# Kernel tuning notes

Hardware: AMD Instinct MI355X
Metric: run time of the kernel (lower is better)

## Reference

```python
import jax, jax.numpy as jnp
import numpy as np

B, C, L = 32, 128, 256  # batch, channels (graph nodes), temporal features (= feas)
K = 2  # Chebyshev order (hardcoded in the module)


def setup_inputs() -> dict:
    key = jax.random.key(0)
    k1, k2, k3 = jax.random.split(key, 3)
    x = jax.random.normal(k1, (B, C, L), dtype=jnp.float32)
    a = jax.random.uniform(k2, (C, C), dtype=jnp.float32)  # nn.Parameter(torch.rand)
    Theta = jax.random.normal(k3, (K, L, L), dtype=jnp.float32)  # (k, feas, num_of_filters)
    return {"x": x, "a": a, "Theta": Theta}


def reference(x, a, Theta):
    b, c, l = x.shape
    # pairwise L1 distance over the feature axis: diff[b,i,j] = sum_l |x[b,i,l] - x[b,j,l]|
    diff = jnp.abs(x[:, :, None, :] - x[:, None, :, :]).sum(-1)  # [b,c,c]
    # F.normalize(diff, dim=0): L2-normalize across the batch dimension
    norm = jnp.sqrt((diff * diff).sum(axis=0, keepdims=True))
    diff = diff / jnp.maximum(norm, 1e-12)
    # learned adjacency
    tmpS = jnp.exp(jax.nn.relu((1.0 - diff) * a))        # [b,c,c]
    adj = tmpS / tmpS.sum(axis=1, keepdims=True)
    deg = adj.sum(axis=1)                                 # [b,c]
    I = jnp.eye(c, dtype=x.dtype)
    D = deg[:, :, None] * I                               # diag_embed(deg)
    Lap = D - adj
    lambda_max = 2.0
    L_t = 2.0 * Lap / lambda_max - I                      # scaled Laplacian, [b,c,c]
    cheb = [jnp.broadcast_to(I, (b, c, c)), L_t]
    for i in range(2, K):
        cheb.append(2.0 * L_t * cheb[i - 1] - cheb[i - 2])
    out = jnp.zeros((b, c, Theta.shape[2]), dtype=x.dtype)
    for kk in range(K):
        # rhs = bmm(T_k^T, x): rhs[b,j,l] = sum_i T_k[b,i,j] * x[b,i,l]
        rhs = jnp.einsum('bij,bil->bjl', cheb[kk], x)
        out = out + rhs @ Theta[kk]
    return jax.nn.relu(out)
```

## Files before the change

### kernel.cpp

```cpp
#include <hip/hip_runtime.h>
#include <hip/hip_bf16.h>


#define NB 32
#define NC 128
#define NL 256

typedef short bf16x8 __attribute__((ext_vector_type(8)));
typedef float f32x4 __attribute__((ext_vector_type(4)));

static __device__ __forceinline__ unsigned short f2bf(float f) {
    unsigned u = __builtin_bit_cast(unsigned, f);
    u += 0x7fff + ((u >> 16) & 1);
    return (unsigned short)(u >> 16);
}

__device__ const unsigned char TI36[36] = {0,0,0,0,0,0,0,0, 1,1,1,1,1,1,1, 2,2,2,2,2,2,
                                           3,3,3,3,3, 4,4,4,4, 5,5,5, 6,6, 7};
__device__ const unsigned char TJ36[36] = {0,1,2,3,4,5,6,7, 1,2,3,4,5,6,7, 2,3,4,5,6,7,
                                           3,4,5,6,7, 4,5,6,7, 5,6,7, 6,7, 7};

__global__ __launch_bounds__(256) void k_pre(const float* __restrict__ x,
                                             const float* __restrict__ Theta,
                                             const float* __restrict__ a,
                                             float* __restrict__ diff,
                                             unsigned short* __restrict__ xb,
                                             unsigned short* __restrict__ thT,
                                             float* __restrict__ aT) {
    __shared__ float smem[8592];
    int bid = blockIdx.x;
    int tid = threadIdx.x;

    if (bid < 1152) {
        int b = bid / 36, p = bid - b * 36;
        int i0 = TI36[p] * 16, j0 = TJ36[p] * 16;
        float* xi = smem;
        float* xj = smem + 4160;
        float* sT = smem + 8320;
        const float4* x4 = (const float4*)(x + (size_t)b * NC * NL);
        for (int idx = tid; idx < 16 * 64; idx += 256) {
            int r = idx >> 6, c = idx & 63;
            *(float4*)&xi[r * 260 + c * 4] = x4[(i0 + r) * 64 + c];
            *(float4*)&xj[r * 260 + c * 4] = x4[(j0 + r) * 64 + c];
        }
        __syncthreads();
        int il = tid >> 4, jl = tid & 15;
        float acc = 0.f;
        #pragma unroll 8
        for (int l4 = 0; l4 < 64; ++l4) {
            float4 u = *(const float4*)&xi[il * 260 + l4 * 4];
            float4 v = *(const float4*)&xj[jl * 260 + l4 * 4];
            acc += fabsf(u.x - v.x) + fabsf(u.y - v.y) +
                   fabsf(u.z - v.z) + fabsf(u.w - v.w);
        }
        float* D = diff + (size_t)b * NC * NC;
        D[(i0 + il) * NC + j0 + jl] = acc;
        sT[jl * 17 + il] = acc;
        __syncthreads();
        D[(j0 + il) * NC + i0 + jl] = sT[il * 17 + jl];
    } else if (bid < 2176) {
        int idx = (bid - 1152) * 256 + tid;
        float4 v = ((const float4*)x)[idx];
        ushort4 o;
        o.x = f2bf(v.x); o.y = f2bf(v.y); o.z = f2bf(v.z); o.w = f2bf(v.w);
        ((ushort4*)xb)[idx] = o;
    } else if (bid < 2208) {
        int tt = bid - 2176;
        int t = tt >> 4, rem = tt & 15;
        int l0 = (rem >> 2) * 64, n0 = (rem & 3) * 64;
        const float* Tp = Theta + (size_t)t * 65536;
        for (int it = tid; it < 4096; it += 256) {
            int r = it >> 6, c = it & 63;
            smem[r * 65 + c] = Tp[(l0 + r) * 256 + n0 + c];
        }
        __syncthreads();
        for (int it = tid; it < 4096; it += 256) {
            int r = it >> 6, c = it & 63;
            thT[(size_t)(t * 256 + n0 + r) * 256 + l0 + c] = f2bf(smem[c * 65 + r]);
        }
    } else {
        int tt = bid - 2208;
        int i0 = (tt >> 1) * 64, j0 = (tt & 1) * 64;
        for (int it = tid; it < 4096; it += 256) {
            int r = it >> 6, c = it & 63;
            smem[r * 65 + c] = a[(i0 + r) * NC + j0 + c];
        }
        __syncthreads();
        for (int it = tid; it < 4096; it += 256) {
            int r = it >> 6, c = it & 63;
            aT[(j0 + r) * NC + i0 + c] = smem[c * 65 + r];
        }
    }
}

__global__ __launch_bounds__(128) void k_adj(const float* __restrict__ diff,
                                             const float* __restrict__ aT,
                                             unsigned short* __restrict__ adjTb) {
    int bid = blockIdx.x;
    int b = bid >> 7, j = bid & 127;
    int i = threadIdx.x;
    const float* Dj = diff + j * NC + i;
    float ss = 0.f;
    #pragma unroll
    for (int bb = 0; bb < NB; ++bb) {
        float v = Dj[(size_t)bb * NC * NC];
        ss = fmaf(v, v, ss);
    }
    float rn = 1.0f / fmaxf(sqrtf(ss), 1e-12f);
    float d  = Dj[(size_t)b * NC * NC];
    float av = aT[j * NC + i];
    float s = __expf(fmaxf((1.0f - d * rn) * av, 0.0f));
    float t = s;
    #pragma unroll
    for (int off = 32; off; off >>= 1) t += __shfl_xor(t, off);
    __shared__ float partial[2];
    if ((i & 63) == 0) partial[i >> 6] = t;
    __syncthreads();
    float total = partial[0] + partial[1];
    adjTb[(size_t)b * NC * NC + j * NC + i] = f2bf(s / total);
}

__global__ __launch_bounds__(256) void k_xth(const unsigned short* __restrict__ xb,
                                             const unsigned short* __restrict__ thT,
                                             float* __restrict__ xTh0,
                                             unsigned short* __restrict__ xTh1T) {
    __shared__ unsigned short Bs[8192];
    int bid = blockIdx.x;
    int mt = bid >> 4, nt = bid & 15;
    int m0 = mt * 128, n0 = nt * 32;
    int tid = threadIdx.x, w = tid >> 6, lane = tid & 63;
    int lr = lane & 15, lg = lane >> 4;

    #pragma unroll
    for (int it = 0; it < 4; ++it) {
        int c = tid + it * 256;
        int n = c >> 5, kc = c & 31;
        bf16x8 v = *(const bf16x8*)(thT + (size_t)(n0 + n) * 256 + kc * 8);
        int dst = n * 512 + ((kc * 16) ^ ((n & 7) << 4));
        *(bf16x8*)((char*)Bs + dst) = v;
    }
    __syncthreads();

    const unsigned short* Ap0 = xb + (size_t)(m0 + w * 32 + lr) * 256 + lg * 8;
    const unsigned short* Ap1 = Ap0 + 16 * 256;
    f32x4 acc00 = {0.f,0.f,0.f,0.f}, acc01 = {0.f,0.f,0.f,0.f};
    f32x4 acc10 = {0.f,0.f,0.f,0.f}, acc11 = {0.f,0.f,0.f,0.f};
    int swz = (lr & 7) << 4;
    #pragma unroll
    for (int ks = 0; ks < 8; ++ks) {
        bf16x8 a0 = *(const bf16x8*)(Ap0 + ks * 32);
        bf16x8 a1 = *(const bf16x8*)(Ap1 + ks * 32);
        int kb = (ks * 64 + lg * 16) ^ swz;
        bf16x8 b0 = *(const bf16x8*)((char*)Bs + lr * 512 + kb);
        bf16x8 b1 = *(const bf16x8*)((char*)Bs + (16 + lr) * 512 + kb);
        acc00 = __builtin_amdgcn_mfma_f32_16x16x32_bf16(a0, b0, acc00, 0, 0, 0);
        acc01 = __builtin_amdgcn_mfma_f32_16x16x32_bf16(a0, b1, acc01, 0, 0, 0);
        acc10 = __builtin_amdgcn_mfma_f32_16x16x32_bf16(a1, b0, acc10, 0, 0, 0);
        acc11 = __builtin_amdgcn_mfma_f32_16x16x32_bf16(a1, b1, acc11, 0, 0, 0);
    }

    int ir0 = w * 32 + lg * 4;
    if (n0 < 256) {
        float* O = xTh0 + (size_t)mt * 32768 + (size_t)ir0 * 256 + n0 + lr;
        #pragma unroll
        for (int r = 0; r < 4; ++r) {
            O[r * 256]              = acc00[r];
            O[r * 256 + 16]         = acc01[r];
            O[(16 + r) * 256]       = acc10[r];
            O[(16 + r) * 256 + 16]  = acc11[r];
        }
    } else {
        int n1 = n0 - 256;
        unsigned short* O = xTh1T + (size_t)mt * 32768;
        ushort4 p;
        p.x = f2bf(acc00[0]); p.y = f2bf(acc00[1]); p.z = f2bf(acc00[2]); p.w = f2bf(acc00[3]);
        *(ushort4*)(O + (size_t)(n1 + lr) * 128 + ir0) = p;
        p.x = f2bf(acc01[0]); p.y = f2bf(acc01[1]); p.z = f2bf(acc01[2]); p.w = f2bf(acc01[3]);
        *(ushort4*)(O + (size_t)(n1 + 16 + lr) * 128 + ir0) = p;
        p.x = f2bf(acc10[0]); p.y = f2bf(acc10[1]); p.z = f2bf(acc10[2]); p.w = f2bf(acc10[3]);
        *(ushort4*)(O + (size_t)(n1 + lr) * 128 + ir0 + 16) = p;
        p.x = f2bf(acc11[0]); p.y = f2bf(acc11[1]); p.z = f2bf(acc11[2]); p.w = f2bf(acc11[3]);
        *(ushort4*)(O + (size_t)(n1 + 16 + lr) * 128 + ir0 + 16) = p;
    }
}

__global__ __launch_bounds__(256) void k_out(const unsigned short* __restrict__ adjTb,
                                             const unsigned short* __restrict__ xTh1T,
                                             const float* __restrict__ xTh0,
                                             float* __restrict__ out) {
    int bid = blockIdx.x;
    int b = bid >> 4, t16 = bid & 15;
    int j0 = (t16 >> 3) * 64, n0 = (t16 & 7) * 32;
    int tid = threadIdx.x, w = tid >> 6, lane = tid & 63;
    int lr = lane & 15, lg = lane >> 4;
    const unsigned short* Ap  = adjTb + (size_t)b * 16384 + (size_t)(j0 + w * 16 + lr) * 128 + lg * 8;
    const unsigned short* Bp0 = xTh1T + (size_t)b * 32768 + (size_t)(n0 + lr) * 128 + lg * 8;
    const unsigned short* Bp1 = Bp0 + 16 * 128;
    f32x4 acc0 = {0.f,0.f,0.f,0.f}, acc1 = {0.f,0.f,0.f,0.f};
    #pragma unroll
    for (int ks = 0; ks < 4; ++ks) {
        bf16x8 av = *(const bf16x8*)(Ap + ks * 32);
        bf16x8 b0 = *(const bf16x8*)(Bp0 + ks * 32);
        bf16x8 b1 = *(const bf16x8*)(Bp1 + ks * 32);
        acc0 = __builtin_amdgcn_mfma_f32_16x16x32_bf16(av, b0, acc0, 0, 0, 0);
        acc1 = __builtin_amdgcn_mfma_f32_16x16x32_bf16(av, b1, acc1, 0, 0, 0);
    }
    int j = j0 + w * 16 + lg * 4;
    const float* X0 = xTh0 + (size_t)b * 32768 + (size_t)j * 256 + n0 + lr;
    float* O = out + (size_t)b * 32768 + (size_t)j * 256 + n0 + lr;
    #pragma unroll
    for (int r = 0; r < 4; ++r) {
        O[r * 256]      = fmaxf(X0[r * 256]      - acc0[r], 0.f);
        O[r * 256 + 16] = fmaxf(X0[r * 256 + 16] - acc1[r], 0.f);
    }
}

extern "C" void kernel_launch(void* const* d_in, const int* in_sizes, int n_in,
                              void* d_out, int out_size, void* d_ws, size_t ws_size,
                              hipStream_t stream) {
    const float* x     = (const float*)d_in[0];
    const float* a     = (const float*)d_in[1];
    const float* Theta = (const float*)d_in[2];
    float* out = (float*)d_out;
    float* f0  = (float*)d_ws;

    float*          diff  = f0;
    unsigned short* xTh1T = (unsigned short*)f0;
    float*          aT    = f0 + 524288;
    float*          xTh0  = f0 + 540672;
    unsigned short* xb    = (unsigned short*)(f0 + 1589248);
    unsigned short* thT   = (unsigned short*)(f0 + 2113536);
    unsigned short* adjTb = (unsigned short*)(f0 + 2179072);

    k_pre<<<dim3(2212), dim3(256), 0, stream>>>(x, Theta, a, diff, xb, thT, aT);
    k_adj<<<dim3(NB * NC), dim3(128), 0, stream>>>(diff, aT, adjTb);
    k_xth<<<dim3(512), dim3(256), 0, stream>>>(xb, thT, xTh0, xTh1T);
    k_out<<<dim3(512), dim3(256), 0, stream>>>(adjTb, xTh1T, xTh0, out);
}
```

Baseline: 92.30 us.

## Fuse all stages into one cooperative persistent kernel with grid syncs

Replaces the four kernel launches with a single cooperative kernel of 512 blocks. It loops over the preprocessing jobs, then separates the adjacency, x·Theta GEMM and output GEMM stages with grid.sync. The per-column batch norm is now computed once into a new rnorm buffer, where each adjacency block used to recompute it by reading all 32 batches of diff. The diff tile load is split into two halves so shared memory fits two blocks per CU. The cost is grid-wide barrier overhead and a fixed grid size, which serialises the preprocessing jobs across blocks.

Result: slower. 335.1 us (+263.0%).

```diff
diff --git a/kernel.cpp b/kernel.cpp
--- a/kernel.cpp
+++ b/kernel.cpp
@@ -1,10 +1,14 @@
 #include <hip/hip_runtime.h>
 #include <hip/hip_bf16.h>
+#include <hip/hip_cooperative_groups.h>
+
+namespace cg = cooperative_groups;
 
 
 #define NB 32
 #define NC 128
 #define NL 256
+#define GRID 512
 
 typedef short bf16x8 __attribute__((ext_vector_type(8)));
 typedef float f32x4 __attribute__((ext_vector_type(4)));
@@ -20,198 +24,209 @@
 __device__ const unsigned char TJ36[36] = {0,1,2,3,4,5,6,7, 1,2,3,4,5,6,7, 2,3,4,5,6,7,
                                            3,4,5,6,7, 4,5,6,7, 5,6,7, 6,7, 7};
 
-__global__ __launch_bounds__(256) void k_pre(const float* __restrict__ x,
-                                             const float* __restrict__ Theta,
-                                             const float* __restrict__ a,
-                                             float* __restrict__ diff,
-                                             unsigned short* __restrict__ xb,
-                                             unsigned short* __restrict__ thT,
-                                             float* __restrict__ aT) {
-    __shared__ float smem[8592];
-    int bid = blockIdx.x;
-    int tid = threadIdx.x;
-
-    if (bid < 1152) {
-        int b = bid / 36, p = bid - b * 36;
-        int i0 = TI36[p] * 16, j0 = TJ36[p] * 16;
-        float* xi = smem;
-        float* xj = smem + 4160;
-        float* sT = smem + 8320;
-        const float4* x4 = (const float4*)(x + (size_t)b * NC * NL);
-        for (int idx = tid; idx < 16 * 64; idx += 256) {
-            int r = idx >> 6, c = idx & 63;
-            *(float4*)&xi[r * 260 + c * 4] = x4[(i0 + r) * 64 + c];
-            *(float4*)&xj[r * 260 + c * 4] = x4[(j0 + r) * 64 + c];
+__global__ __launch_bounds__(256, 2) void k_fused(
+    const float* __restrict__ x, const float* __restrict__ Theta, const float* __restrict__ a,
+    float* __restrict__ diff, unsigned short* __restrict__ xb, unsigned short* __restrict__ thT,
+    float* __restrict__ aT, float* __restrict__ rnorm, unsigned short* __restrict__ adjTb,
+    float* __restrict__ xTh0, unsigned short* __restrict__ xTh1T, float* __restrict__ out)
+{
+    cg::grid_group grid = cg::this_grid();
+    __shared__ __align__(16) float smem[4496];
+    __shared__ float partial[4];
+    int bid = blockIdx.x, tid = threadIdx.x;
+
+    for (int job = bid; job < 2212; job += GRID) {
+        if (job < 1152) {
+            int b = job / 36, p = job - b * 36;
+            int i0 = TI36[p] * 16, j0 = TJ36[p] * 16;
+            float* xi = smem;
+            float* xj = smem + 2112;
+            float* sT = smem + 4224;
+            const float4* x4 = (const float4*)(x + (size_t)b * NC * NL);
+            int il = tid >> 4, jl = tid & 15;
+            float acc = 0.f;
+            #pragma unroll
+            for (int h = 0; h < 2; ++h) {
+                __syncthreads();
+                for (int idx = tid; idx < 512; idx += 256) {
+                    int r = idx >> 5, c = idx & 31;
+                    *(float4*)&xi[r * 132 + c * 4] = x4[(i0 + r) * 64 + h * 32 + c];
+                    *(float4*)&xj[r * 132 + c * 4] = x4[(j0 + r) * 64 + h * 32 + c];
+                }
+                __syncthreads();
+                #pragma unroll 8
+                for (int l4 = 0; l4 < 32; ++l4) {
+                    float4 u = *(const float4*)&xi[il * 132 + l4 * 4];
+                    float4 v = *(const float4*)&xj[jl * 132 + l4 * 4];
+                    acc += fabsf(u.x - v.x) + fabsf(u.y - v.y) +
+                           fabsf(u.z - v.z) + fabsf(u.w - v.w);
+                }
+            }
+            float* D = diff + (size_t)b * NC * NC;
+            D[(i0 + il) * NC + j0 + jl] = acc;
+            __syncthreads();
+            sT[jl * 17 + il] = acc;
+            __syncthreads();
+            D[(j0 + il) * NC + i0 + jl] = sT[il * 17 + jl];
+        } else if (job < 2176) {
+            int idx = (job - 1152) * 256 + tid;
+            float4 v = ((const float4*)x)[idx];
+            ushort4 o;
+            o.x = f2bf(v.x); o.y = f2bf(v.y); o.z = f2bf(v.z); o.w = f2bf(v.w);
+            ((ushort4*)xb)[idx] = o;
+        } else if (job < 2208) {
+            int tt = job - 2176;
+            int t = tt >> 4, rem = tt & 15;
+            int l0 = (rem >> 2) * 64, n0 = (rem & 3) * 64;
+            const float* Tp = Theta + (size_t)t * 65536;
+            __syncthreads();
+            for (int it = tid; it < 4096; it += 256) {
+                int r = it >> 6, c = it & 63;
+                smem[r * 65 + c] = Tp[(l0 + r) * 256 + n0 + c];
+            }
+            __syncthreads();
+            for (int it = tid; it < 4096; it += 256) {
+                int r = it >> 6, c = it & 63;
+                thT[(size_t)(t * 256 + n0 + r) * 256 + l0 + c] = f2bf(smem[c * 65 + r]);
+            }
+        } else {
+            int tt = job - 2208;
+            int i0 = (tt >> 1) * 64, j0 = (tt & 1) * 64;
+            __syncthreads();
+            for (int it = tid; it < 4096; it += 256) {
+                int r = it >> 6, c = it & 63;
+                smem[r * 65 + c] = a[(i0 + r) * NC + j0 + c];
+            }
+            __syncthreads();
+            for (int it = tid; it < 4096; it += 256) {
+                int r = it >> 6, c = it & 63;
+                aT[(j0 + r) * NC + i0 + c] = smem[c * 65 + r];
+            }
+        }
+    }
+    grid.sync();
+
+    if (bid < 64) {
+        int idx = bid * 256 + tid;
+        float ss = 0.f;
+        #pragma unroll
+        for (int bb = 0; bb < NB; ++bb) {
+            float v = diff[(size_t)bb * NC * NC + idx];
+            ss = fmaf(v, v, ss);
+        }
+        rnorm[idx] = 1.0f / fmaxf(sqrtf(ss), 1e-12f);
+    }
+    grid.sync();
+
+    {
+        int g = tid >> 7;
+        int i = tid & 127;
+        #pragma unroll
+        for (int it = 0; it < 4; ++it) {
+            __syncthreads();
+            int P = it * 1024 + bid * 2 + g;
+            int b = P >> 7, j = P & 127;
+            float d  = diff[(size_t)b * NC * NC + j * NC + i];
+            float rn = rnorm[j * NC + i];
+            float av = aT[j * NC + i];
+            float s = __expf(fmaxf((1.0f - d * rn) * av, 0.0f));
+            float t = s;
+            #pragma unroll
+            for (int off = 32; off; off >>= 1) t += __shfl_xor(t, off);
+            if ((tid & 63) == 0) partial[tid >> 6] = t;
+            __syncthreads();
+            float total = partial[g << 1] + partial[(g << 1) | 1];
+            adjTb[(size_t)b * NC * NC + j * NC + i] = f2bf(s / total);
+        }
+    }
+    grid.sync();
+
+    {
+        unsigned short* Bs = (unsigned short*)smem;
+        int mt = bid >> 4, nt = bid & 15;
+        int m0 = mt * 128, n0 = nt * 32;
+        int w = tid >> 6, lane = tid & 63;
+        int lr = lane & 15, lg = lane >> 4;
+
+        #pragma unroll
+        for (int it = 0; it < 4; ++it) {
+            int c = tid + it * 256;
+            int n = c >> 5, kc = c & 31;
+            bf16x8 v = *(const bf16x8*)(thT + (size_t)(n0 + n) * 256 + kc * 8);
+            int dst = n * 512 + ((kc * 16) ^ ((n & 7) << 4));
+            *(bf16x8*)((char*)Bs + dst) = v;
         }
         __syncthreads();
-        int il = tid >> 4, jl = tid & 15;
-        float acc = 0.f;
-        #pragma unroll 8
-        for (int l4 = 0; l4 < 64; ++l4) {
-            float4 u = *(const float4*)&xi[il * 260 + l4 * 4];
-            float4 v = *(const float4*)&xj[jl * 260 + l4 * 4];
-            acc += fabsf(u.x - v.x) + fabsf(u.y - v.y) +
-                   fabsf(u.z - v.z) + fabsf(u.w - v.w);
-        }
-        float* D = diff + (size_t)b * NC * NC;
-        D[(i0 + il) * NC + j0 + jl] = acc;
-        sT[jl * 17 + il] = acc;
-        __syncthreads();
-        D[(j0 + il) * NC + i0 + jl] = sT[il * 17 + jl];
-    } else if (bid < 2176) {
-        int idx = (bid - 1152) * 256 + tid;
-        float4 v = ((const float4*)x)[idx];
-        ushort4 o;
-        o.x = f2bf(v.x); o.y = f2bf(v.y); o.z = f2bf(v.z); o.w = f2bf(v.w);
-        ((ushort4*)xb)[idx] = o;
-    } else if (bid < 2208) {
-        int tt = bid - 2176;
-        int t = tt >> 4, rem = tt & 15;
-        int l0 = (rem >> 2) * 64, n0 = (rem & 3) * 64;
-        const float* Tp = Theta + (size_t)t * 65536;
-        for (int it = tid; it < 4096; it += 256) {
-            int r = it >> 6, c = it & 63;
-            smem[r * 65 + c] = Tp[(l0 + r) * 256 + n0 + c];
-        }
-        __syncthreads();
-        for (int it = tid; it < 4096; it += 256) {
-            int r = it >> 6, c = it & 63;
-            thT[(size_t)(t * 256 + n0 + r) * 256 + l0 + c] = f2bf(smem[c * 65 + r]);
-        }
-    } else {
-        int tt = bid - 2208;
-        int i0 = (tt >> 1) * 64, j0 = (tt & 1) * 64;
-        for (int it = tid; it < 4096; it += 256) {
-            int r = it >> 6, c = it & 63;
-            smem[r * 65 + c] = a[(i0 + r) * NC + j0 + c];
-        }
-        __syncthreads();
-        for (int it = tid; it < 4096; it += 256) {
-            int r = it >> 6, c = it & 63;
-            aT[(j0 + r) * NC + i0 + c] = smem[c * 65 + r];
-        }
-    }
-}
-
-__global__ __launch_bounds__(128) void k_adj(const float* __restrict__ diff,
-                                             const float* __restrict__ aT,
-                                             unsigned short* __restrict__ adjTb) {
-    int bid = blockIdx.x;
-    int b = bid >> 7, j = bid & 127;
-    int i = threadIdx.x;
-    const float* Dj = diff + j * NC + i;
-    float ss = 0.f;
-    #pragma unroll
-    for (int bb = 0; bb < NB; ++bb) {
-        float v = Dj[(size_t)bb * NC * NC];
-        ss = fmaf(v, v, ss);
-    }
-    float rn = 1.0f / fmaxf(sqrtf(ss), 1e-12f);
-    float d  = Dj[(size_t)b * NC * NC];
-    float av = aT[j * NC + i];
-    float s = __expf(fmaxf((1.0f - d * rn) * av, 0.0f));
-    float t = s;
-    #pragma unroll
-    for (int off = 32; off; off >>= 1) t += __shfl_xor(t, off);
-    __shared__ float partial[2];
-    if ((i & 63) == 0) partial[i >> 6] = t;
-    __syncthreads();
-    float total = partial[0] + partial[1];
-    adjTb[(size_t)b * NC * NC + j * NC + i] = f2bf(s / total);
-}
-
-__global__ __launch_bounds__(256) void k_xth(const unsigned short* __restrict__ xb,
-                                             const unsigned short* __restrict__ thT,
-                                             float* __restrict__ xTh0,
-                                             unsigned short* __restrict__ xTh1T) {
-    __shared__ unsigned short Bs[8192];
-    int bid = blockIdx.x;
-    int mt = bid >> 4, nt = bid & 15;
-    int m0 = mt * 128, n0 = nt * 32;
-    int tid = threadIdx.x, w = tid >> 6, lane = tid & 63;
-    int lr = lane & 15, lg = lane >> 4;
-
-    #pragma unroll
-    for (int it = 0; it < 4; ++it) {
-        int c = tid + it * 256;
-        int n = c >> 5, kc = c & 31;
-        bf16x8 v = *(const bf16x8*)(thT + (size_t)(n0 + n) * 256 + kc * 8);
-        int dst = n * 512 + ((kc * 16) ^ ((n & 7) << 4));
-        *(bf16x8*)((char*)Bs + dst) = v;
-    }
-    __syncthreads();
-
-    const unsigned short* Ap0 = xb + (size_t)(m0 + w * 32 + lr) * 256 + lg * 8;
-    const unsigned short* Ap1 = Ap0 + 16 * 256;
-    f32x4 acc00 = {0.f,0.f,0.f,0.f}, acc01 = {0.f,0.f,0.f,0.f};
-    f32x4 acc10 = {0.f,0.f,0.f,0.f}, acc11 = {0.f,0.f,0.f,0.f};
-    int swz = (lr & 7) << 4;
-    #pragma unroll
-    for (int ks = 0; ks < 8; ++ks) {
-        bf16x8 a0 = *(const bf16x8*)(Ap0 + ks * 32);
-        bf16x8 a1 = *(const bf16x8*)(Ap1 + ks * 32);
-        int kb = (ks * 64 + lg * 16) ^ swz;
-        bf16x8 b0 = *(const bf16x8*)((char*)Bs + lr * 512 + kb);
-        bf16x8 b1 = *(const bf16x8*)((char*)Bs + (16 + lr) * 512 + kb);
-        acc00 = __builtin_amdgcn_mfma_f32_16x16x32_bf16(a0, b0, acc00, 0, 0, 0);
-        acc01 = __builtin_amdgcn_mfma_f32_16x16x32_bf16(a0, b1, acc01, 0, 0, 0);
-        acc10 = __builtin_amdgcn_mfma_f32_16x16x32_bf16(a1, b0, acc10, 0, 0, 0);
-        acc11 = __builtin_amdgcn_mfma_f32_16x16x32_bf16(a1, b1, acc11, 0, 0, 0);
-    }
-
-    int ir0 = w * 32 + lg * 4;
-    if (n0 < 256) {
-        float* O = xTh0 + (size_t)mt * 32768 + (size_t)ir0 * 256 + n0 + lr;
+
+        const unsigned short* Ap0 = xb + (size_t)(m0 + w * 32 + lr) * 256 + lg * 8;
+        const unsigned short* Ap1 = Ap0 + 16 * 256;
+        f32x4 acc00 = {0.f,0.f,0.f,0.f}, acc01 = {0.f,0.f,0.f,0.f};
+        f32x4 acc10 = {0.f,0.f,0.f,0.f}, acc11 = {0.f,0.f,0.f,0.f};
+        int swz = (lr & 7) << 4;
+        #pragma unroll
+        for (int ks = 0; ks < 8; ++ks) {
+            bf16x8 a0 = *(const bf16x8*)(Ap0 + ks * 32);
+            bf16x8 a1 = *(const bf16x8*)(Ap1 + ks * 32);
+            int kb = (ks * 64 + lg * 16) ^ swz;
+            bf16x8 b0 = *(const bf16x8*)((char*)Bs + lr * 512 + kb);
+            bf16x8 b1 = *(const bf16x8*)((char*)Bs + (16 + lr) * 512 + kb);
+            acc00 = __builtin_amdgcn_mfma_f32_16x16x32_bf16(a0, b0, acc00, 0, 0, 0);
+            acc01 = __builtin_amdgcn_mfma_f32_16x16x32_bf16(a0, b1, acc01, 0, 0, 0);
+            acc10 = __builtin_amdgcn_mfma_f32_16x16x32_bf16(a1, b0, acc10, 0, 0, 0);
+            acc11 = __builtin_amdgcn_mfma_f32_16x16x32_bf16(a1, b1, acc11, 0, 0, 0);
+        }
+
+        int ir0 = w * 32 + lg * 4;
+        if (n0 < 256) {
+            float* O = xTh0 + (size_t)mt * 32768 + (size_t)ir0 * 256 + n0 + lr;
+            #pragma unroll
+            for (int r = 0; r < 4; ++r) {
+                O[r * 256]              = acc00[r];
+                O[r * 256 + 16]         = acc01[r];
+                O[(16 + r) * 256]       = acc10[r];
+                O[(16 + r) * 256 + 16]  = acc11[r];
+            }
+        } else {
+            int n1 = n0 - 256;
+            unsigned short* O = xTh1T + (size_t)mt * 32768;
+            ushort4 p;
+            p.x = f2bf(acc00[0]); p.y = f2bf(acc00[1]); p.z = f2bf(acc00[2]); p.w = f2bf(acc00[3]);
+            *(ushort4*)(O + (size_t)(n1 + lr) * 128 + ir0) = p;
+            p.x = f2bf(acc01[0]); p.y = f2bf(acc01[1]); p.z = f2bf(acc01[2]); p.w = f2bf(acc01[3]);
+            *(ushort4*)(O + (size_t)(n1 + 16 + lr) * 128 + ir0) = p;
+            p.x = f2bf(acc10[0]); p.y = f2bf(acc10[1]); p.z = f2bf(acc10[2]); p.w = f2bf(acc10[3]);
+            *(ushort4*)(O + (size_t)(n1 + lr) * 128 + ir0 + 16) = p;
+            p.x = f2bf(acc11[0]); p.y = f2bf(acc11[1]); p.z = f2bf(acc11[2]); p.w = f2bf(acc11[3]);
+            *(ushort4*)(O + (size_t)(n1 + 16 + lr) * 128 + ir0 + 16) = p;
+        }
+    }
+    grid.sync();
+
+    {
+        int b = bid >> 4, t16 = bid & 15;
+        int j0 = (t16 >> 3) * 64, n0 = (t16 & 7) * 32;
+        int w = tid >> 6, lane = tid & 63;
+        int lr = lane & 15, lg = lane >> 4;
+        const unsigned short* Ap  = adjTb + (size_t)b * 16384 + (size_t)(j0 + w * 16 + lr) * 128 + lg * 8;
+        const unsigned short* Bp0 = xTh1T + (size_t)b * 32768 + (size_t)(n0 + lr) * 128 + lg * 8;
+        const unsigned short* Bp1 = Bp0 + 16 * 128;
+        f32x4 acc0 = {0.f,0.f,0.f,0.f}, acc1 = {0.f,0.f,0.f,0.f};
+        #pragma unroll
+        for (int ks = 0; ks < 4; ++ks) {
+            bf16x8 av = *(const bf16x8*)(Ap + ks * 32);
+            bf16x8 b0 = *(const bf16x8*)(Bp0 + ks * 32);
+            bf16x8 b1 = *(const bf16x8*)(Bp1 + ks * 32);
+            acc0 = __builtin_amdgcn_mfma_f32_16x16x32_bf16(av, b0, acc0, 0, 0, 0);
+            acc1 = __builtin_amdgcn_mfma_f32_16x16x32_bf16(av, b1, acc1, 0, 0, 0);
+        }
+        int j = j0 + w * 16 + lg * 4;
+        const float* X0 = xTh0 + (size_t)b * 32768 + (size_t)j * 256 + n0 + lr;
+        float* O = out + (size_t)b * 32768 + (size_t)j * 256 + n0 + lr;
         #pragma unroll
         for (int r = 0; r < 4; ++r) {
-            O[r * 256]              = acc00[r];
-            O[r * 256 + 16]         = acc01[r];
-            O[(16 + r) * 256]       = acc10[r];
-            O[(16 + r) * 256 + 16]  = acc11[r];
-        }
-    } else {
-        int n1 = n0 - 256;
-        unsigned short* O = xTh1T + (size_t)mt * 32768;
-        ushort4 p;
-        p.x = f2bf(acc00[0]); p.y = f2bf(acc00[1]); p.z = f2bf(acc00[2]); p.w = f2bf(acc00[3]);
-        *(ushort4*)(O + (size_t)(n1 + lr) * 128 + ir0) = p;
-        p.x = f2bf(acc01[0]); p.y = f2bf(acc01[1]); p.z = f2bf(acc01[2]); p.w = f2bf(acc01[3]);
-        *(ushort4*)(O + (size_t)(n1 + 16 + lr) * 128 + ir0) = p;
-        p.x = f2bf(acc10[0]); p.y = f2bf(acc10[1]); p.z = f2bf(acc10[2]); p.w = f2bf(acc10[3]);
-        *(ushort4*)(O + (size_t)(n1 + lr) * 128 + ir0 + 16) = p;
-        p.x = f2bf(acc11[0]); p.y = f2bf(acc11[1]); p.z = f2bf(acc11[2]); p.w = f2bf(acc11[3]);
-        *(ushort4*)(O + (size_t)(n1 + 16 + lr) * 128 + ir0 + 16) = p;
-    }
-}
-
-__global__ __launch_bounds__(256) void k_out(const unsigned short* __restrict__ adjTb,
-                                             const unsigned short* __restrict__ xTh1T,
-                                             const float* __restrict__ xTh0,
-                                             float* __restrict__ out) {
-    int bid = blockIdx.x;
-    int b = bid >> 4, t16 = bid & 15;
-    int j0 = (t16 >> 3) * 64, n0 = (t16 & 7) * 32;
-    int tid = threadIdx.x, w = tid >> 6, lane = tid & 63;
-    int lr = lane & 15, lg = lane >> 4;
-    const unsigned short* Ap  = adjTb + (size_t)b * 16384 + (size_t)(j0 + w * 16 + lr) * 128 + lg * 8;
-    const unsigned short* Bp0 = xTh1T + (size_t)b * 32768 + (size_t)(n0 + lr) * 128 + lg * 8;
-    const unsigned short* Bp1 = Bp0 + 16 * 128;
-    f32x4 acc0 = {0.f,0.f,0.f,0.f}, acc1 = {0.f,0.f,0.f,0.f};
-    #pragma unroll
-    for (int ks = 0; ks < 4; ++ks) {
-        bf16x8 av = *(const bf16x8*)(Ap + ks * 32);
-        bf16x8 b0 = *(const bf16x8*)(Bp0 + ks * 32);
-        bf16x8 b1 = *(const bf16x8*)(Bp1 + ks * 32);
-        acc0 = __builtin_amdgcn_mfma_f32_16x16x32_bf16(av, b0, acc0, 0, 0, 0);
-        acc1 = __builtin_amdgcn_mfma_f32_16x16x32_bf16(av, b1, acc1, 0, 0, 0);
-    }
-    int j = j0 + w * 16 + lg * 4;
-    const float* X0 = xTh0 + (size_t)b * 32768 + (size_t)j * 256 + n0 + lr;
-    float* O = out + (size_t)b * 32768 + (size_t)j * 256 + n0 + lr;
-    #pragma unroll
-    for (int r = 0; r < 4; ++r) {
-        O[r * 256]      = fmaxf(X0[r * 256]      - acc0[r], 0.f);
-        O[r * 256 + 16] = fmaxf(X0[r * 256 + 16] - acc1[r], 0.f);
+            O[r * 256]      = fmaxf(X0[r * 256]      - acc0[r], 0.f);
+            O[r * 256 + 16] = fmaxf(X0[r * 256 + 16] - acc1[r], 0.f);
+        }
     }
 }
 
@@ -227,13 +242,14 @@
     float*          diff  = f0;
     unsigned short* xTh1T = (unsigned short*)f0;
     float*          aT    = f0 + 524288;
-    float*          xTh0  = f0 + 540672;
-    unsigned short* xb    = (unsigned short*)(f0 + 1589248);
-    unsigned short* thT   = (unsigned short*)(f0 + 2113536);
-    unsigned short* adjTb = (unsigned short*)(f0 + 2179072);
-
-    k_pre<<<dim3(2212), dim3(256), 0, stream>>>(x, Theta, a, diff, xb, thT, aT);
-    k_adj<<<dim3(NB * NC), dim3(128), 0, stream>>>(diff, aT, adjTb);
-    k_xth<<<dim3(512), dim3(256), 0, stream>>>(xb, thT, xTh0, xTh1T);
-    k_out<<<dim3(512), dim3(256), 0, stream>>>(adjTb, xTh1T, xTh0, out);
+    float*          rnorm = f0 + 540672;
+    float*          xTh0  = f0 + 557056;
+    unsigned short* xb    = (unsigned short*)(f0 + 1605632);
+    unsigned short* thT   = (unsigned short*)(f0 + 2129920);
+    unsigned short* adjTb = (unsigned short*)(f0 + 2195456);
+
+    void* args[] = {(void*)&x, (void*)&Theta, (void*)&a, (void*)&diff, (void*)&xb,
+                    (void*)&thT, (void*)&aT, (void*)&rnorm, (void*)&adjTb,
+                    (void*)&xTh0, (void*)&xTh1T, (void*)&out};
+    hipLaunchCooperativeKernel((const void*)k_fused, dim3(GRID), dim3(256), args, 0, stream);
 }
```

## Fuse adjacency, propagation and Theta GEMMs into one kernel with reordered matmul

Applied to the files above, without the earlier changes.

Replaces the adjacency, x·Theta and output kernels with a single kernel per (batch, 16-row tile). The kernel computes the normalized adjacency in registers and LDS, forms y = adjᵀx first, then runs one K=512 GEMM of [x | y] against a stacked Theta. The sign and the identity term are folded into the negated adjacency. The preprocessing kernel now also emits a transposed bf16 x and a stacked transposed Theta. This removes intermediate global round-trips and two launches, at the cost of recomputing the batch L2 norm in every tile and launching only 256 blocks.

After: 99.55 us. +7.9%, slower.

```diff
diff --git a/kernel.cpp b/kernel.cpp
--- a/kernel.cpp
+++ b/kernel.cpp
@@ -25,7 +25,8 @@
                                              const float* __restrict__ a,
                                              float* __restrict__ diff,
                                              unsigned short* __restrict__ xb,
-                                             unsigned short* __restrict__ thT,
+                                             unsigned short* __restrict__ xbT,
+                                             unsigned short* __restrict__ thT2,
                                              float* __restrict__ aT) {
     __shared__ float smem[8592];
     int bid = blockIdx.x;
@@ -58,28 +59,52 @@
         sT[jl * 17 + il] = acc;
         __syncthreads();
         D[(j0 + il) * NC + i0 + jl] = sT[il * 17 + jl];
-    } else if (bid < 2176) {
-        int idx = (bid - 1152) * 256 + tid;
-        float4 v = ((const float4*)x)[idx];
-        ushort4 o;
-        o.x = f2bf(v.x); o.y = f2bf(v.y); o.z = f2bf(v.z); o.w = f2bf(v.w);
-        ((ushort4*)xb)[idx] = o;
-    } else if (bid < 2208) {
-        int tt = bid - 2176;
+    } else if (bid < 1408) {
+        int tt = bid - 1152;
+        int b = tt >> 3, rem = tt & 7;
+        int i0 = (rem >> 2) * 64, l0 = (rem & 3) * 64;
+        const float4* x4 = (const float4*)(x + (size_t)b * NC * NL);
+        for (int idx = tid; idx < 1024; idx += 256) {
+            int r = idx >> 4, c4 = idx & 15;
+            *(float4*)&smem[r * 65 + c4 * 4] = x4[(i0 + r) * 64 + (l0 >> 2) + c4];
+        }
+        __syncthreads();
+        for (int idx = tid; idx < 1024; idx += 256) {
+            int r = idx >> 4, c4 = idx & 15;
+            ushort4 o;
+            o.x = f2bf(smem[r * 65 + c4 * 4 + 0]);
+            o.y = f2bf(smem[r * 65 + c4 * 4 + 1]);
+            o.z = f2bf(smem[r * 65 + c4 * 4 + 2]);
+            o.w = f2bf(smem[r * 65 + c4 * 4 + 3]);
+            *(ushort4*)(xb + (size_t)b * 32768 + (size_t)(i0 + r) * 256 + l0 + c4 * 4) = o;
+            ushort4 p;
+            p.x = f2bf(smem[(c4 * 4 + 0) * 65 + r]);
+            p.y = f2bf(smem[(c4 * 4 + 1) * 65 + r]);
+            p.z = f2bf(smem[(c4 * 4 + 2) * 65 + r]);
+            p.w = f2bf(smem[(c4 * 4 + 3) * 65 + r]);
+            *(ushort4*)(xbT + (size_t)b * 32768 + (size_t)(l0 + r) * 128 + i0 + c4 * 4) = p;
+        }
+    } else if (bid < 1440) {
+        int tt = bid - 1408;
         int t = tt >> 4, rem = tt & 15;
         int l0 = (rem >> 2) * 64, n0 = (rem & 3) * 64;
-        const float* Tp = Theta + (size_t)t * 65536;
-        for (int it = tid; it < 4096; it += 256) {
-            int r = it >> 6, c = it & 63;
-            smem[r * 65 + c] = Tp[(l0 + r) * 256 + n0 + c];
-        }
-        __syncthreads();
-        for (int it = tid; it < 4096; it += 256) {
-            int r = it >> 6, c = it & 63;
-            thT[(size_t)(t * 256 + n0 + r) * 256 + l0 + c] = f2bf(smem[c * 65 + r]);
+        const float4* T4 = (const float4*)(Theta + (size_t)t * 65536);
+        for (int idx = tid; idx < 1024; idx += 256) {
+            int r = idx >> 4, c4 = idx & 15;
+            *(float4*)&smem[r * 65 + c4 * 4] = T4[(l0 + r) * 64 + (n0 >> 2) + c4];
+        }
+        __syncthreads();
+        for (int idx = tid; idx < 1024; idx += 256) {
+            int r = idx >> 4, c4 = idx & 15;
+            ushort4 o;
+            o.x = f2bf(smem[(c4 * 4 + 0) * 65 + r]);
+            o.y = f2bf(smem[(c4 * 4 + 1) * 65 + r]);
+            o.z = f2bf(smem[(c4 * 4 + 2) * 65 + r]);
+            o.w = f2bf(smem[(c4 * 4 + 3) * 65 + r]);
+            *(ushort4*)(thT2 + (size_t)(n0 + r) * 512 + t * 256 + l0 + c4 * 4) = o;
         }
     } else {
-        int tt = bid - 2208;
+        int tt = bid - 1440;
         int i0 = (tt >> 1) * 64, j0 = (tt & 1) * 64;
         for (int it = tid; it < 4096; it += 256) {
             int r = it >> 6, c = it & 63;
@@ -93,125 +118,95 @@
     }
 }
 
-__global__ __launch_bounds__(128) void k_adj(const float* __restrict__ diff,
-                                             const float* __restrict__ aT,
-                                             unsigned short* __restrict__ adjTb) {
+__global__ __launch_bounds__(256) void k_mega(const float* __restrict__ diff,
+                                              const float* __restrict__ aT,
+                                              const unsigned short* __restrict__ xb,
+                                              const unsigned short* __restrict__ xbT,
+                                              const unsigned short* __restrict__ thT2,
+                                              float* __restrict__ out) {
+    __shared__ __align__(16) short adjL[16 * 144];
+    __shared__ __align__(16) short yL[16 * 272];
     int bid = blockIdx.x;
-    int b = bid >> 7, j = bid & 127;
-    int i = threadIdx.x;
-    const float* Dj = diff + j * NC + i;
-    float ss = 0.f;
-    #pragma unroll
-    for (int bb = 0; bb < NB; ++bb) {
-        float v = Dj[(size_t)bb * NC * NC];
-        ss = fmaf(v, v, ss);
-    }
-    float rn = 1.0f / fmaxf(sqrtf(ss), 1e-12f);
-    float d  = Dj[(size_t)b * NC * NC];
-    float av = aT[j * NC + i];
-    float s = __expf(fmaxf((1.0f - d * rn) * av, 0.0f));
-    float t = s;
-    #pragma unroll
-    for (int off = 32; off; off >>= 1) t += __shfl_xor(t, off);
-    __shared__ float partial[2];
-    if ((i & 63) == 0) partial[i >> 6] = t;
+    int b = bid >> 3, jt = bid & 7, j0 = jt * 16;
+    int tid = threadIdx.x;
+
+    {
+        int jl = tid >> 4, il = tid & 15;
+        const float* Dp = diff + (size_t)(j0 + jl) * NC + il;
+        const float* Ap = aT + (size_t)(j0 + jl) * NC + il;
+        float sv[8];
+        float cs = 0.f;
+        #pragma unroll
+        for (int r = 0; r < 8; ++r) {
+            int off = 16 * r;
+            float ss = 0.f;
+            #pragma unroll
+            for (int bb = 0; bb < NB; ++bb) {
+                float v = Dp[(size_t)bb * NC * NC + off];
+                ss = fmaf(v, v, ss);
+            }
+            float rn = 1.0f / fmaxf(sqrtf(ss), 1e-12f);
+            float d  = Dp[(size_t)b * NC * NC + off];
+            float av = Ap[off];
+            float s = __expf(fmaxf((1.0f - d * rn) * av, 0.0f));
+            sv[r] = s;
+            cs += s;
+        }
+        cs += __shfl_xor(cs, 1); cs += __shfl_xor(cs, 2);
+        cs += __shfl_xor(cs, 4); cs += __shfl_xor(cs, 8);
+        float inv = -1.0f / cs;
+        #pragma unroll
+        for (int r = 0; r < 8; ++r)
+            adjL[jl * 144 + il + 16 * r] = (short)f2bf(sv[r] * inv);
+    }
     __syncthreads();
-    float total = partial[0] + partial[1];
-    adjTb[(size_t)b * NC * NC + j * NC + i] = f2bf(s / total);
-}
-
-__global__ __launch_bounds__(256) void k_xth(const unsigned short* __restrict__ xb,
-                                             const unsigned short* __restrict__ thT,
-                                             float* __restrict__ xTh0,
-                                             unsigned short* __restrict__ xTh1T) {
-    __shared__ unsigned short Bs[8192];
-    int bid = blockIdx.x;
-    int mt = bid >> 4, nt = bid & 15;
-    int m0 = mt * 128, n0 = nt * 32;
-    int tid = threadIdx.x, w = tid >> 6, lane = tid & 63;
-    int lr = lane & 15, lg = lane >> 4;
-
-    #pragma unroll
-    for (int it = 0; it < 4; ++it) {
-        int c = tid + it * 256;
-        int n = c >> 5, kc = c & 31;
-        bf16x8 v = *(const bf16x8*)(thT + (size_t)(n0 + n) * 256 + kc * 8);
-        int dst = n * 512 + ((kc * 16) ^ ((n & 7) << 4));
-        *(bf16x8*)((char*)Bs + dst) = v;
+
+    int w = tid >> 6, lane = tid & 63, lr = lane & 15, lg = lane >> 4;
+
+    {
+        f32x4 acc[4];
+        #pragma unroll
+        for (int f = 0; f < 4; ++f) acc[f] = (f32x4){0.f, 0.f, 0.f, 0.f};
+        const unsigned short* Bb = xbT + (size_t)b * 32768;
+        #pragma unroll
+        for (int ks = 0; ks < 4; ++ks) {
+            bf16x8 af = *(const bf16x8*)&adjL[lr * 144 + ks * 32 + lg * 8];
+            #pragma unroll
+            for (int f = 0; f < 4; ++f) {
+                bf16x8 bv = *(const bf16x8*)(Bb + (size_t)(w * 64 + f * 16 + lr) * 128 + ks * 32 + lg * 8);
+                acc[f] = __builtin_amdgcn_mfma_f32_16x16x32_bf16(af, bv, acc[f], 0, 0, 0);
+            }
+        }
+        #pragma unroll
+        for (int f = 0; f < 4; ++f)
+            #pragma unroll
+            for (int r = 0; r < 4; ++r)
+                yL[(lg * 4 + r) * 272 + w * 64 + f * 16 + lr] = (short)f2bf(acc[f][r]);
     }
     __syncthreads();
 
-    const unsigned short* Ap0 = xb + (size_t)(m0 + w * 32 + lr) * 256 + lg * 8;
-    const unsigned short* Ap1 = Ap0 + 16 * 256;
-    f32x4 acc00 = {0.f,0.f,0.f,0.f}, acc01 = {0.f,0.f,0.f,0.f};
-    f32x4 acc10 = {0.f,0.f,0.f,0.f}, acc11 = {0.f,0.f,0.f,0.f};
-    int swz = (lr & 7) << 4;
-    #pragma unroll
-    for (int ks = 0; ks < 8; ++ks) {
-        bf16x8 a0 = *(const bf16x8*)(Ap0 + ks * 32);
-        bf16x8 a1 = *(const bf16x8*)(Ap1 + ks * 32);
-        int kb = (ks * 64 + lg * 16) ^ swz;
-        bf16x8 b0 = *(const bf16x8*)((char*)Bs + lr * 512 + kb);
-        bf16x8 b1 = *(const bf16x8*)((char*)Bs + (16 + lr) * 512 + kb);
-        acc00 = __builtin_amdgcn_mfma_f32_16x16x32_bf16(a0, b0, acc00, 0, 0, 0);
-        acc01 = __builtin_amdgcn_mfma_f32_16x16x32_bf16(a0, b1, acc01, 0, 0, 0);
-        acc10 = __builtin_amdgcn_mfma_f32_16x16x32_bf16(a1, b0, acc10, 0, 0, 0);
-        acc11 = __builtin_amdgcn_mfma_f32_16x16x32_bf16(a1, b1, acc11, 0, 0, 0);
-    }
-
-    int ir0 = w * 32 + lg * 4;
-    if (n0 < 256) {
-        float* O = xTh0 + (size_t)mt * 32768 + (size_t)ir0 * 256 + n0 + lr;
-        #pragma unroll
-        for (int r = 0; r < 4; ++r) {
-            O[r * 256]              = acc00[r];
-            O[r * 256 + 16]         = acc01[r];
-            O[(16 + r) * 256]       = acc10[r];
-            O[(16 + r) * 256 + 16]  = acc11[r];
-        }
-    } else {
-        int n1 = n0 - 256;
-        unsigned short* O = xTh1T + (size_t)mt * 32768;
-        ushort4 p;
-        p.x = f2bf(acc00[0]); p.y = f2bf(acc00[1]); p.z = f2bf(acc00[2]); p.w = f2bf(acc00[3]);
-        *(ushort4*)(O + (size_t)(n1 + lr) * 128 + ir0) = p;
-        p.x = f2bf(acc01[0]); p.y = f2bf(acc01[1]); p.z = f2bf(acc01[2]); p.w = f2bf(acc01[3]);
-        *(ushort4*)(O + (size_t)(n1 + 16 + lr) * 128 + ir0) = p;
-        p.x = f2bf(acc10[0]); p.y = f2bf(acc10[1]); p.z = f2bf(acc10[2]); p.w = f2bf(acc10[3]);
-        *(ushort4*)(O + (size_t)(n1 + lr) * 128 + ir0 + 16) = p;
-        p.x = f2bf(acc11[0]); p.y = f2bf(acc11[1]); p.z = f2bf(acc11[2]); p.w = f2bf(acc11[3]);
-        *(ushort4*)(O + (size_t)(n1 + 16 + lr) * 128 + ir0 + 16) = p;
-    }
-}
-
-__global__ __launch_bounds__(256) void k_out(const unsigned short* __restrict__ adjTb,
-                                             const unsigned short* __restrict__ xTh1T,
-                                             const float* __restrict__ xTh0,
-                                             float* __restrict__ out) {
-    int bid = blockIdx.x;
-    int b = bid >> 4, t16 = bid & 15;
-    int j0 = (t16 >> 3) * 64, n0 = (t16 & 7) * 32;
-    int tid = threadIdx.x, w = tid >> 6, lane = tid & 63;
-    int lr = lane & 15, lg = lane >> 4;
-    const unsigned short* Ap  = adjTb + (size_t)b * 16384 + (size_t)(j0 + w * 16 + lr) * 128 + lg * 8;
-    const unsigned short* Bp0 = xTh1T + (size_t)b * 32768 + (size_t)(n0 + lr) * 128 + lg * 8;
-    const unsigned short* Bp1 = Bp0 + 16 * 128;
-    f32x4 acc0 = {0.f,0.f,0.f,0.f}, acc1 = {0.f,0.f,0.f,0.f};
-    #pragma unroll
-    for (int ks = 0; ks < 4; ++ks) {
-        bf16x8 av = *(const bf16x8*)(Ap + ks * 32);
-        bf16x8 b0 = *(const bf16x8*)(Bp0 + ks * 32);
-        bf16x8 b1 = *(const bf16x8*)(Bp1 + ks * 32);
-        acc0 = __builtin_amdgcn_mfma_f32_16x16x32_bf16(av, b0, acc0, 0, 0, 0);
-        acc1 = __builtin_amdgcn_mfma_f32_16x16x32_bf16(av, b1, acc1, 0, 0, 0);
-    }
-    int j = j0 + w * 16 + lg * 4;
-    const float* X0 = xTh0 + (size_t)b * 32768 + (size_t)j * 256 + n0 + lr;
-    float* O = out + (size_t)b * 32768 + (size_t)j * 256 + n0 + lr;
-    #pragma unroll
-    for (int r = 0; r < 4; ++r) {
-        O[r * 256]      = fmaxf(X0[r * 256]      - acc0[r], 0.f);
-        O[r * 256 + 16] = fmaxf(X0[r * 256 + 16] - acc1[r], 0.f);
+    {
+        f32x4 o[4];
+        #pragma unroll
+        for (int f = 0; f < 4; ++f) o[f] = (f32x4){0.f, 0.f, 0.f, 0.f};
+        const unsigned short* Arow = xb + (size_t)b * 32768 + (size_t)(j0 + lr) * 256;
+        #pragma unroll
+        for (int ks = 0; ks < 16; ++ks) {
+            bf16x8 af = (ks < 8)
+                ? *(const bf16x8*)(Arow + ks * 32 + lg * 8)
+                : *(const bf16x8*)&yL[lr * 272 + (ks - 8) * 32 + lg * 8];
+            #pragma unroll
+            for (int f = 0; f < 4; ++f) {
+                bf16x8 bv = *(const bf16x8*)(thT2 + (size_t)(w * 64 + f * 16 + lr) * 512 + ks * 32 + lg * 8);
+                o[f] = __builtin_amdgcn_mfma_f32_16x16x32_bf16(af, bv, o[f], 0, 0, 0);
+            }
+        }
+        float* Ob = out + (size_t)b * 32768;
+        #pragma unroll
+        for (int f = 0; f < 4; ++f)
+            #pragma unroll
+            for (int r = 0; r < 4; ++r)
+                Ob[(size_t)(j0 + lg * 4 + r) * 256 + w * 64 + f * 16 + lr] = fmaxf(o[f][r], 0.f);
     }
 }
 
@@ -224,16 +219,12 @@
     float* out = (float*)d_out;
     float* f0  = (float*)d_ws;
 
-    float*          diff  = f0;
-    unsigned short* xTh1T = (unsigned short*)f0;
-    float*          aT    = f0 + 524288;
-    float*          xTh0  = f0 + 540672;
-    unsigned short* xb    = (unsigned short*)(f0 + 1589248);
-    unsigned short* thT   = (unsigned short*)(f0 + 2113536);
-    unsigned short* adjTb = (unsigned short*)(f0 + 2179072);
-
-    k_pre<<<dim3(2212), dim3(256), 0, stream>>>(x, Theta, a, diff, xb, thT, aT);
-    k_adj<<<dim3(NB * NC), dim3(128), 0, stream>>>(diff, aT, adjTb);
-    k_xth<<<dim3(512), dim3(256), 0, stream>>>(xb, thT, xTh0, xTh1T);
-    k_out<<<dim3(512), dim3(256), 0, stream>>>(adjTb, xTh1T, xTh0, out);
-}
+    float*          diff = f0;
+    float*          aT   = f0 + 524288;
+    unsigned short* xb   = (unsigned short*)(f0 + 540672);
+    unsigned short* xbT  = (unsigned short*)(f0 + 1064960);
+    unsigned short* thT2 = (unsigned short*)(f0 + 1589248);
+
+    k_pre <<<dim3(1444), dim3(256), 0, stream>>>(x, Theta, a, diff, xb, xbT, thT2, aT);
+    k_mega<<<dim3(256), dim3(256), 0, stream>>>(diff, aT, xb, xbT, thT2, out);
+}
```
